# Kernel optimization log

Hardware: AMD Instinct MI355X
Metric: run time of the kernel (lower is better)

## Reference

```python
import jax, jax.numpy as jnp
import numpy as np

ALPHA = 1.0
ARAP_WEIGHT = 1.0
B, N, K, LATENT, HIDDEN = 16, 20000, 16, 256, 1024


def setup_inputs() -> dict:
    key = jax.random.key(0)
    ks = jax.random.split(key, 8)
    code = jax.random.normal(ks[0], (B, LATENT), jnp.float32)
    W1 = jax.random.normal(ks[1], (LATENT, HIDDEN), jnp.float32) / np.sqrt(LATENT)
    b1 = jnp.zeros((HIDDEN,), jnp.float32)
    W2 = jax.random.normal(ks[2], (HIDDEN, N * 3), jnp.float32) / np.sqrt(HIDDEN)
    b2 = jnp.zeros((N * 3,), jnp.float32)
    xyz1 = jax.random.normal(ks[3], (B, N, 3), jnp.float32)
    weightMatrix = jax.random.uniform(ks[4], (N, K), jnp.float32)
    area = jax.random.uniform(ks[5], (N,), jnp.float32)
    neighborsMatrix = jax.random.randint(ks[6], (N, K), 0, N, jnp.int32)
    numNeighbors = jax.random.randint(ks[7], (N,), 1, K + 1, jnp.int32)
    return {"code": code, "W1": W1, "b1": b1, "W2": W2, "b2": b2,
            "xyz1": xyz1, "weightMatrix": weightMatrix, "area": area,
            "neighborsMatrix": neighborsMatrix, "numNeighbors": numNeighbors}


def _mean_energy(code, W1, b1, W2, b2, xyz1, weightMatrix, area,
                 neighborsMatrix, numNeighbors):
    # decoder: MLP latent -> hidden -> N*3, reshaped to [B,N,3]
    h = jax.nn.relu(code @ W1 + b1)
    recon = (h @ W2 + b2).reshape(B, N, 3)

    # mask out padded neighbor slots, fold into weights  [N,K]
    mask = (jnp.arange(K)[None, :] < numNeighbors[:, None]).astype(jnp.float32)
    wm = weightMatrix * mask

    # neighbor-gathered edge vectors: rest pose d, deformed dq  [B,N,K,3]
    d = xyz1[:, :, None, :] - xyz1[:, neighborsMatrix, :]
    dq = recon[:, :, None, :] - recon[:, neighborsMatrix, :]

    # per-vertex weighted covariance and best-fit rotation (Procrustes)
    S = jnp.einsum('nk,bnki,bnkj->bnij', wm, d, dq)          # [B,N,3,3]
    U, s, Vt = jnp.linalg.svd(S)
    V = jnp.swapaxes(Vt, -1, -2)
    Ut = jnp.swapaxes(U, -1, -2)
    det = jnp.linalg.det(V @ Ut)                              # [B,N]
    Vf = V.at[..., :, -1].multiply(jnp.sign(det)[..., None])  # reflection fix
    R = jax.lax.stop_gradient(Vf @ Ut)                        # R treated as constant

    resid = dq - jnp.einsum('bnij,bnkj->bnki', R, d)          # [B,N,K,3]
    e = (ARAP_WEIGHT * ALPHA) * area[None, :, None] * wm[None] \
        * jnp.sum(resid * resid, axis=-1)                     # [B,N,K]
    # torch.mean(torch.mean(e, 2), 1)
    return jnp.mean(e, axis=(1, 2))                           # [B]


def reference(code, W1, b1, W2, b2, xyz1, weightMatrix, area,
              neighborsMatrix, numNeighbors):
    meanEnergy = _mean_energy(code, W1, b1, W2, b2, xyz1, weightMatrix, area,
                              neighborsMatrix, numNeighbors)
    # meanEnergy.backward(ones) -> grad of sum(meanEnergy) wrt code
    code_grad = jax.grad(lambda c: jnp.sum(
        _mean_energy(c, W1, b1, W2, b2, xyz1, weightMatrix, area,
                     neighborsMatrix, numNeighbors)))(code)
    return (meanEnergy, code_grad)
```

## Files before the change

### kernel.cpp

```cpp
#include <hip/hip_runtime.h>

constexpr int B_ = 16;
constexpr int NV = 20000;
constexpr int KN = 16;
constexpr int LAT = 256;
constexpr int HID = 1024;
constexpr int N3 = 60000;
constexpr int RCAP = 64;
constexpr int NCHUNK = 8;
constexpr float INV_NK = 1.0f / (20000.0f * 16.0f);

constexpr size_t H_OFF      = 0;
constexpr size_t XQ_OFF     = H_OFF + B_ * HID;
constexpr size_t GRECON_OFF = XQ_OFF + (size_t)NV * 96;
constexpr size_t GH_OFF     = GRECON_OFF + (size_t)B_ * N3;
constexpr size_t OWNG_OFF   = GH_OFF + B_ * HID;
constexpr size_t GEDGE_OFF  = OWNG_OFF + (size_t)NV * 64;
constexpr size_t RCOUNT_OFF = GEDGE_OFF + (size_t)NV * KN * 64;
constexpr size_t RLIST_OFF  = RCOUNT_OFF + NV;
constexpr size_t PART_OFF   = RLIST_OFF + (size_t)NV * RCAP;

__device__ __forceinline__ void atomAddF(float* p, float v) {
  unsafeAtomicAdd(p, v);
}

__global__ __launch_bounds__(256) void k_prep(
    const float* __restrict__ xyz, const float* __restrict__ code,
    const float* __restrict__ W1, const float* __restrict__ b1,
    float* __restrict__ xq, float* __restrict__ h,
    float* __restrict__ gh, float* __restrict__ out,
    int* __restrict__ rcount) {
  const int bid = blockIdx.x, tid = threadIdx.x;
  if (bid < 938) {
    __shared__ float sm[64][17];
    const int n30 = bid * 64;
    {
      const int n3l = tid & 63, bq = tid >> 6;
      #pragma unroll
      for (int p = 0; p < 4; ++p) {
        int b = p * 4 + bq;
        if (n30 + n3l < N3) sm[n3l][b] = xyz[(size_t)b * N3 + n30 + n3l];
      }
    }
    __syncthreads();
    {
      const int b = tid & 15, nq = tid >> 4;
      #pragma unroll
      for (int p = 0; p < 4; ++p) {
        int n3 = n30 + p * 16 + nq;
        if (n3 < N3) {
          int n = n3 / 3, c = n3 - n * 3;
          xq[(size_t)n * 96 + c * 16 + b] = sm[p * 16 + nq][b];
        }
      }
    }
  } else if (bid < 1002) {
    int t = (bid - 938) * 256 + tid;
    int b = t >> 10, hd = t & 1023;
    const float* c = code + b * LAT;
    float acc = b1[hd];
    #pragma unroll 4
    for (int l = 0; l < LAT; ++l) acc += c[l] * W1[l * HID + hd];
    h[t] = fmaxf(acc, 0.0f);
  } else if (bid < 1006) {
    int base = (bid - 1002) * 4096 + tid;
    #pragma unroll
    for (int r = 0; r < 16; ++r) gh[base + r * 256] = 0.0f;
  } else if (bid == 1006) {
    for (int i = tid; i < B_ + B_ * LAT; i += 256) out[i] = 0.0f;
  } else {
    int i = (bid - 1007) * 256 + tid;
    if (i < NV) rcount[i] = 0;
  }
}

__global__ __launch_bounds__(256) void k_mlp2f(
    const float* __restrict__ h, const float* __restrict__ W2,
    float* __restrict__ part,
    const int* __restrict__ nbrs, const int* __restrict__ nnbr,
    int* __restrict__ rcount, int* __restrict__ rlist) {
  const int bid = blockIdx.x;
  const int tid = threadIdx.x;
  if (bid >= 472) {
    int e = (bid - 472) * 256 + tid;
    int n = e >> 4, k = e & 15;
    if (k < nnbr[n]) {
      int v = nbrs[e];
      int slot = atomicAdd(&rcount[v], 1);
      if (slot < RCAP) rlist[v * RCAP + slot] = e;
    }
    return;
  }
  const int bx = bid % 59, by = bid / 59;
  __shared__ float hs[16][128];
  const int hd0 = by * 128;
  #pragma unroll
  for (int r = 0; r < 8; ++r) {
    int idx = r * 256 + tid;
    int bb = idx >> 7, cc = idx & 127;
    hs[bb][cc] = h[bb * HID + hd0 + cc];
  }
  __syncthreads();

  const int j4 = bx * 1024 + tid * 4;
  if (j4 >= N3) return;

  float4 acc[16];
  #pragma unroll
  for (int b = 0; b < 16; ++b) acc[b] = make_float4(0.f, 0.f, 0.f, 0.f);

  const float* wp = W2 + (size_t)hd0 * N3 + j4;
  float4 w0 = *(const float4*)(wp);
  float4 w1 = *(const float4*)(wp + (size_t)N3);
  float4 w2 = *(const float4*)(wp + (size_t)2 * N3);
  float4 w3 = *(const float4*)(wp + (size_t)3 * N3);

  for (int g = 0; g < 32; ++g) {
    const float* np = wp + (size_t)4 * N3;
    float4 n0, n1, n2, n3;
    if (g < 31) {
      n0 = *(const float4*)(np);
      n1 = *(const float4*)(np + (size_t)N3);
      n2 = *(const float4*)(np + (size_t)2 * N3);
      n3 = *(const float4*)(np + (size_t)3 * N3);
    }
    #pragma unroll
    for (int b = 0; b < 16; ++b) {
      float4 hb = *(const float4*)&hs[b][g * 4];
      acc[b].x += hb.x * w0.x + hb.y * w1.x + hb.z * w2.x + hb.w * w3.x;
      acc[b].y += hb.x * w0.y + hb.y * w1.y + hb.z * w2.y + hb.w * w3.y;
      acc[b].z += hb.x * w0.z + hb.y * w1.z + hb.z * w2.z + hb.w * w3.z;
      acc[b].w += hb.x * w0.w + hb.y * w1.w + hb.z * w2.w + hb.w * w3.w;
    }
    wp = np; w0 = n0; w1 = n1; w2 = n2; w3 = n3;
  }

  float ac[4][16];
  #pragma unroll
  for (int b = 0; b < 16; ++b) {
    ac[0][b] = acc[b].x; ac[1][b] = acc[b].y;
    ac[2][b] = acc[b].z; ac[3][b] = acc[b].w;
  }
  float* pbase = part + ((size_t)by * N3 + j4) * 16;
  #pragma unroll
  for (int jj = 0; jj < 4; ++jj)
    #pragma unroll
    for (int q = 0; q < 4; ++q)
      *(float4*)(pbase + jj * 16 + q * 4) = make_float4(
          ac[jj][q*4+0], ac[jj][q*4+1], ac[jj][q*4+2], ac[jj][q*4+3]);
}

__global__ __launch_bounds__(256) void k_reduce(
    const float* __restrict__ part, const float* __restrict__ b2,
    float* __restrict__ xq) {
  int t = blockIdx.x * 256 + threadIdx.x;
  if (t >= N3 * 16 / 4) return;
  size_t pos = (size_t)t * 4;
  int j = t >> 2, bq = (t & 3) * 4;
  float4 s = *(const float4*)(part + pos);
  #pragma unroll
  for (int c = 1; c < NCHUNK; ++c) {
    float4 p = *(const float4*)(part + (size_t)c * N3 * 16 + pos);
    s.x += p.x; s.y += p.y; s.z += p.z; s.w += p.w;
  }
  float bias = b2[j];
  s.x += bias; s.y += bias; s.z += bias; s.w += bias;
  int n = j / 3, c = j - n * 3;
  *(float4*)(xq + (size_t)n * 96 + (3 + c) * 16 + bq) = s;
}

__global__ __launch_bounds__(256, 2) void k_rot(
    const float* __restrict__ xq,
    const float* __restrict__ wmat, const float* __restrict__ area,
    const int* __restrict__ nbrs, const int* __restrict__ nnbr,
    float* __restrict__ ownG, float* __restrict__ gEdge,
    float* __restrict__ energy) {
  __shared__ float red[64];
  const int tid = threadIdx.x;
  const int b = tid & 15, nl = tid >> 4;
  const int n = blockIdx.x * 16 + nl;
  const int nn = nnbr[n];
  const float ar = area[n];
  const float* xqn = xq + (size_t)n * 96 + b;
  const float x0 = xqn[0],  x1 = xqn[16], x2 = xqn[32];
  const float q0 = xqn[48], q1 = xqn[64], q2 = xqn[80];

  float dX[KN], dY[KN], dZ[KN], eX[KN], eY[KN], eZ[KN], wk[KN];
  float S00=0,S01=0,S02=0,S10=0,S11=0,S12=0,S20=0,S21=0,S22=0;
  #pragma unroll
  for (int k = 0; k < KN; ++k) {
    float w=0, dx=0, dy=0, dz=0, ex=0, ey=0, ez=0;
    if (k < nn) {
      int m = nbrs[n * KN + k];
      w = wmat[n * KN + k];
      const float* mp = xq + (size_t)m * 96 + b;
      dx = x0 - mp[0];  dy = x1 - mp[16]; dz = x2 - mp[32];
      ex = q0 - mp[48]; ey = q1 - mp[64]; ez = q2 - mp[80];
    }
    wk[k]=w; dX[k]=dx; dY[k]=dy; dZ[k]=dz; eX[k]=ex; eY[k]=ey; eZ[k]=ez;
    S00 += w*dx*ex; S01 += w*dx*ey; S02 += w*dx*ez;
    S10 += w*dy*ex; S11 += w*dy*ey; S12 += w*dy*ez;
    S20 += w*dz*ex; S21 += w*dz*ey; S22 += w*dz*ez;
  }

  float A00 = S00*S00 + S10*S10 + S20*S20;
  float A01 = S00*S01 + S10*S11 + S20*S21;
  float A02 = S00*S02 + S10*S12 + S20*S22;
  float A11 = S01*S01 + S11*S11 + S21*S21;
  float A12 = S01*S02 + S11*S12 + S21*S22;
  float A22 = S02*S02 + S12*S12 + S22*S22;
  float V00=1,V01=0,V02=0, V10=0,V11=1,V12=0, V20=0,V21=0,V22=1;

  auto rot = [&](float& app, float& aqq, float& apq, float& arp, float& arq,
                 float& vp0, float& vp1, float& vp2,
                 float& vq0, float& vq1, float& vq2) {
    float a = apq;
    if (fabsf(a) > 1e-37f) {
      float tau = (aqq - app) * 0.5f / a;
      float t = copysignf(1.0f, tau) / (fabsf(tau) + sqrtf(1.0f + tau * tau));
      float c = rsqrtf(1.0f + t * t);
      float s = t * c;
      float napp = c*c*app - 2.0f*s*c*a + s*s*aqq;
      float naqq = s*s*app + 2.0f*s*c*a + c*c*aqq;
      app = napp; aqq = naqq; apq = 0.0f;
      float rp = arp, rq = arq;
      arp = c*rp - s*rq; arq = s*rp + c*rq;
      float t0, t1;
      t0=vp0; t1=vq0; vp0 = c*t0 - s*t1; vq0 = s*t0 + c*t1;
      t0=vp1; t1=vq1; vp1 = c*t0 - s*t1; vq1 = s*t0 + c*t1;
      t0=vp2; t1=vq2; vp2 = c*t0 - s*t1; vq2 = s*t0 + c*t1;
    }
  };
  #pragma unroll
  for (int sweep = 0; sweep < 6; ++sweep) {
    rot(A00,A11,A01, A02,A12, V00,V10,V20, V01,V11,V21);
    rot(A00,A22,A02, A01,A12, V00,V10,V20, V02,V12,V22);
    rot(A11,A22,A12, A01,A02, V01,V11,V21, V02,V12,V22);
  }
  auto sw = [](float& a, float& c) { float t = a; a = c; c = t; };
  if (A00 < A11) { sw(A00,A11); sw(V00,V01); sw(V10,V11); sw(V20,V21); }
  if (A00 < A22) { sw(A00,A22); sw(V00,V02); sw(V10,V12); sw(V20,V22); }
  if (A11 < A22) { sw(A11,A22); sw(V01,V02); sw(V11,V12); sw(V21,V22); }

  float v1x=V00, v1y=V10, v1z=V20;
  float v2x=V01, v2y=V11, v2z=V21;

  float u1x = S00*v1x + S01*v1y + S02*v1z;
  float u1y = S10*v1x + S11*v1y + S12*v1z;
  float u1z = S20*v1x + S21*v1y + S22*v1z;
  float s1sq = u1x*u1x + u1y*u1y + u1z*u1z;
  if (s1sq > 1e-30f) { float r = rsqrtf(s1sq); u1x*=r; u1y*=r; u1z*=r; }
  else { u1x = 1.0f; u1y = 0.0f; u1z = 0.0f; }

  float u2x = S00*v2x + S01*v2y + S02*v2z;
  float u2y = S10*v2x + S11*v2y + S12*v2z;
  float u2z = S20*v2x + S21*v2y + S22*v2z;
  float pr = u2x*u1x + u2y*u1y + u2z*u1z;
  u2x -= pr*u1x; u2y -= pr*u1y; u2z -= pr*u1z;
  float s2sq = u2x*u2x + u2y*u2y + u2z*u2z;
  if (s2sq > 1e-12f * s1sq + 1e-30f) {
    float r = rsqrtf(s2sq); u2x*=r; u2y*=r; u2z*=r;
  } else {
    float ex_ = (fabsf(u1x) < 0.9f) ? 1.0f : 0.0f;
    float ey_ = 1.0f - ex_;
    float pp = ex_*u1x + ey_*u1y;
    u2x = ex_ - pp*u1x; u2y = ey_ - pp*u1y; u2z = -pp*u1z;
    float r = rsqrtf(u2x*u2x + u2y*u2y + u2z*u2z);
    u2x*=r; u2y*=r; u2z*=r;
  }
  float u3x = u1y*u2z - u1z*u2y, u3y = u1z*u2x - u1x*u2z, u3z = u1x*u2y - u1y*u2x;
  float v3x = v1y*v2z - v1z*v2y, v3y = v1z*v2x - v1x*v2z, v3z = v1x*v2y - v1y*v2x;

  float R00 = v1x*u1x + v2x*u2x + v3x*u3x;
  float R01 = v1x*u1y + v2x*u2y + v3x*u3y;
  float R02 = v1x*u1z + v2x*u2z + v3x*u3z;
  float R10 = v1y*u1x + v2y*u2x + v3y*u3x;
  float R11 = v1y*u1y + v2y*u2y + v3y*u3y;
  float R12 = v1y*u1z + v2y*u2z + v3y*u3z;
  float R20 = v1z*u1x + v2z*u2x + v3z*u3x;
  float R21 = v1z*u1y + v2z*u2y + v3z*u3y;
  float R22 = v1z*u1z + v2z*u2z + v3z*u3z;

  float esum = 0, go0 = 0, go1 = 0, go2 = 0;
  const float gf = 2.0f * ar * INV_NK;
  float* geb = gEdge + (size_t)n * 1024 + b * 4;
  #pragma unroll
  for (int k = 0; k < KN; ++k) {
    float w = wk[k];
    float dx = dX[k], dy = dY[k], dz = dZ[k];
    float rx = eX[k] - (R00*dx + R01*dy + R02*dz);
    float ry = eY[k] - (R10*dx + R11*dy + R12*dz);
    float rz = eZ[k] - (R20*dx + R21*dy + R22*dz);
    esum += w * (rx*rx + ry*ry + rz*rz);
    float gc = gf * w;
    float gx = gc*rx, gy = gc*ry, gz = gc*rz;
    go0 += gx; go1 += gy; go2 += gz;
    if (k < nn) {
      *(float4*)(geb + k * 64) = make_float4(gx, gy, gz, 0.0f);
    }
  }
  esum *= ar * INV_NK;

  *(float4*)(ownG + (size_t)n * 64 + b * 4) = make_float4(go0, go1, go2, 0.0f);

  esum += __shfl_down(esum, 32);
  esum += __shfl_down(esum, 16);
  int wave = tid >> 6, lane = tid & 63;
  if (lane < 16) red[wave * 16 + lane] = esum;
  __syncthreads();
  if (tid < 16) atomAddF(&energy[tid], red[tid] + red[16 + tid] + red[32 + tid] + red[48 + tid]);
}

__global__ __launch_bounds__(256) void k_scatter(
    const float* __restrict__ gEdge, const float* __restrict__ ownG,
    const int* __restrict__ rcount, const int* __restrict__ rlist,
    float* __restrict__ grecon) {
  int t = blockIdx.x * 256 + threadIdx.x;
  int v = t >> 4, b = t & 15;
  const float4 og = *(const float4*)(ownG + (size_t)v * 64 + b * 4);
  float g0 = og.x, g1 = og.y, g2 = og.z;
  int deg = min(rcount[v], RCAP);
  const int* rl = rlist + v * RCAP;
  int i = 0;
  for (; i + 3 < deg; i += 4) {
    int e0 = rl[i], e1 = rl[i + 1], e2 = rl[i + 2], e3 = rl[i + 3];
    float4 p0 = *(const float4*)(gEdge + (size_t)e0 * 64 + b * 4);
    float4 p1 = *(const float4*)(gEdge + (size_t)e1 * 64 + b * 4);
    float4 p2 = *(const float4*)(gEdge + (size_t)e2 * 64 + b * 4);
    float4 p3 = *(const float4*)(gEdge + (size_t)e3 * 64 + b * 4);
    g0 -= (p0.x + p1.x) + (p2.x + p3.x);
    g1 -= (p0.y + p1.y) + (p2.y + p3.y);
    g2 -= (p0.z + p1.z) + (p2.z + p3.z);
  }
  for (; i < deg; ++i) {
    int e = rl[i];
    float4 p = *(const float4*)(gEdge + (size_t)e * 64 + b * 4);
    g0 -= p.x; g1 -= p.y; g2 -= p.z;
  }
  float* gq = grecon + (size_t)b * N3 + v * 3;
  gq[0] = g0; gq[1] = g1; gq[2] = g2;
}

__global__ __launch_bounds__(256, 2) void k_mlp2_bwd(
    const float* __restrict__ gr, const float* __restrict__ W2,
    float* __restrict__ gh) {
  const int tid = threadIdx.x;
  const int lane = tid & 63;
  const int wv = tid >> 6;
  const int laneJ = lane & 15, laneR = lane >> 4;
  const int row0 = blockIdx.y * 32 + wv * 8 + laneR * 2;

  float4 acc0[16], acc1[16];
  #pragma unroll
  for (int b = 0; b < 16; ++b) {
    acc0[b] = make_float4(0.f, 0.f, 0.f, 0.f);
    acc1[b] = make_float4(0.f, 0.f, 0.f, 0.f);
  }

  const int jbase = blockIdx.x * 64 + laneJ * 4;
  const float* w2r0 = W2 + (size_t)row0 * N3;
  const float* w2r1 = w2r0 + N3;

  for (int it = 0; it < 15; ++it) {
    int j = jbase + it * 4096;
    if (j < N3) {
      float4 w0 = *(const float4*)(w2r0 + j);
      float4 w1 = *(const float4*)(w2r1 + j);
      #pragma unroll
      for (int b = 0; b < 16; ++b) {
        float4 g = *(const float4*)(gr + (size_t)b * N3 + j);
        acc0[b].x += g.x * w0.x; acc0[b].y += g.y * w0.y;
        acc0[b].z += g.z * w0.z; acc0[b].w += g.w * w0.w;
        acc1[b].x += g.x * w1.x; acc1[b].y += g.y * w1.y;
        acc1[b].z += g.z * w1.z; acc1[b].w += g.w * w1.w;
      }
    }
  }

  float s0[16], s1[16];
  #pragma unroll
  for (int b = 0; b < 16; ++b) {
    s0[b] = (acc0[b].x + acc0[b].y) + (acc0[b].z + acc0[b].w);
    s1[b] = (acc1[b].x + acc1[b].y) + (acc1[b].z + acc1[b].w);
  }
  #pragma unroll
  for (int m = 1; m <= 8; m <<= 1) {
    #pragma unroll
    for (int b = 0; b < 16; ++b) {
      s0[b] += __shfl_xor(s0[b], m);
      s1[b] += __shfl_xor(s1[b], m);
    }
  }
  if (laneJ == 0) {
    #pragma unroll
    for (int b = 0; b < 16; ++b) {
      atomAddF(&gh[b * HID + row0], s0[b]);
      atomAddF(&gh[b * HID + row0 + 1], s1[b]);
    }
  }
}

__global__ __launch_bounds__(256) void k_mlp1_bwd(
    const float* __restrict__ gh, const float* __restrict__ h,
    const float* __restrict__ W1, float* __restrict__ gcode) {
  __shared__ float gm[128];
  const int b = blockIdx.x;
  const int hd0 = blockIdx.y * 128;
  const int l = threadIdx.x;
  if (l < 128) {
    float g = gh[b * HID + hd0 + l];
    gm[l] = (h[b * HID + hd0 + l] > 0.0f) ? g : 0.0f;
  }
  __syncthreads();
  const float4* wp = (const float4*)(W1 + (size_t)l * HID + hd0);
  float acc = 0.0f;
  #pragma unroll
  for (int i = 0; i < 32; ++i) {
    float4 w4 = wp[i];
    acc += w4.x * gm[i*4+0] + w4.y * gm[i*4+1] + w4.z * gm[i*4+2] + w4.w * gm[i*4+3];
  }
  atomAddF(&gcode[b * LAT + l], acc);
}

extern "C" void kernel_launch(void* const* d_in, const int* in_sizes, int n_in,
                              void* d_out, int out_size, void* d_ws, size_t ws_size,
                              hipStream_t stream) {
  const float* code = (const float*)d_in[0];
  const float* W1   = (const float*)d_in[1];
  const float* b1   = (const float*)d_in[2];
  const float* W2   = (const float*)d_in[3];
  const float* b2   = (const float*)d_in[4];
  const float* xyz  = (const float*)d_in[5];
  const float* wmat = (const float*)d_in[6];
  const float* area = (const float*)d_in[7];
  const int* nbrs   = (const int*)d_in[8];
  const int* nnbr   = (const int*)d_in[9];

  float* out = (float*)d_out;
  float* ws = (float*)d_ws;
  float* h      = ws + H_OFF;
  float* xq     = ws + XQ_OFF;
  float* grecon = ws + GRECON_OFF;
  float* gh     = ws + GH_OFF;
  float* ownG   = ws + OWNG_OFF;
  float* gEdge  = ws + GEDGE_OFF;
  int*   rcount = (int*)(ws + RCOUNT_OFF);
  int*   rlist  = (int*)(ws + RLIST_OFF);
  float* part   = ws + PART_OFF;

  k_prep<<<dim3(1086), dim3(256), 0, stream>>>(xyz, code, W1, b1, xq, h, gh, out, rcount);
  k_mlp2f<<<dim3(472 + NV * KN / 256), dim3(256), 0, stream>>>(
      h, W2, part, nbrs, nnbr, rcount, rlist);
  k_reduce<<<dim3((N3 * 16 / 4 + 255) / 256), dim3(256), 0, stream>>>(part, b2, xq);
  k_rot<<<dim3(NV / 16), dim3(256), 0, stream>>>(
      xq, wmat, area, nbrs, nnbr, ownG, gEdge, out);
  k_scatter<<<dim3(NV * 16 / 256), dim3(256), 0, stream>>>(
      gEdge, ownG, rcount, rlist, grecon);
  k_mlp2_bwd<<<dim3(64, 32), dim3(256), 0, stream>>>(grecon, W2, gh);
  k_mlp1_bwd<<<dim3(B_, 8), dim3(256), 0, stream>>>(gh, h, W1, out + B_);
}
```

Measured before the change: 617.4 us.

## Transpose recon gradient layout and remap MLP2 backward work per lane

The scatter kernel now writes the recon gradient as [N3][16] (batch innermost) instead of [B][N3]. The MLP2 backward kernel is rewritten so each lane owns one batch index and a strip of 8 j-values. Each lane accumulates into 8 W2 rows with a short cross-lane reduction, replacing 128 float4 accumulators with 8 scalars. The aim is lower register pressure and fewer shuffles and atomics, at the cost of less-coalesced W2 reads (each lane loads 32 contiguous bytes per row).

```diff
diff --git a/kernel.cpp b/kernel.cpp
--- a/kernel.cpp
+++ b/kernel.cpp
@@ -12,8 +12,8 @@
 
 constexpr size_t H_OFF      = 0;
 constexpr size_t XQ_OFF     = H_OFF + B_ * HID;
-constexpr size_t GRECON_OFF = XQ_OFF + (size_t)NV * 96;
-constexpr size_t GH_OFF     = GRECON_OFF + (size_t)B_ * N3;
+constexpr size_t GRT_OFF    = XQ_OFF + (size_t)NV * 96;
+constexpr size_t GH_OFF     = GRT_OFF + (size_t)N3 * 16;
 constexpr size_t OWNG_OFF   = GH_OFF + B_ * HID;
 constexpr size_t GEDGE_OFF  = OWNG_OFF + (size_t)NV * 64;
 constexpr size_t RCOUNT_OFF = GEDGE_OFF + (size_t)NV * KN * 64;
@@ -314,7 +314,7 @@
 __global__ __launch_bounds__(256) void k_scatter(
     const float* __restrict__ gEdge, const float* __restrict__ ownG,
     const int* __restrict__ rcount, const int* __restrict__ rlist,
-    float* __restrict__ grecon) {
+    float* __restrict__ grT) {
   int t = blockIdx.x * 256 + threadIdx.x;
   int v = t >> 4, b = t & 15;
   const float4 og = *(const float4*)(ownG + (size_t)v * 64 + b * 4);
@@ -337,66 +337,51 @@
     float4 p = *(const float4*)(gEdge + (size_t)e * 64 + b * 4);
     g0 -= p.x; g1 -= p.y; g2 -= p.z;
   }
-  float* gq = grecon + (size_t)b * N3 + v * 3;
-  gq[0] = g0; gq[1] = g1; gq[2] = g2;
-}
-
-__global__ __launch_bounds__(256, 2) void k_mlp2_bwd(
-    const float* __restrict__ gr, const float* __restrict__ W2,
+  float* gq = grT + (size_t)v * 48 + b;
+  gq[0] = g0; gq[16] = g1; gq[32] = g2;
+}
+
+__global__ __launch_bounds__(256) void k_mlp2_bwd(
+    const float* __restrict__ grT, const float* __restrict__ W2,
     float* __restrict__ gh) {
   const int tid = threadIdx.x;
   const int lane = tid & 63;
-  const int wv = tid >> 6;
-  const int laneJ = lane & 15, laneR = lane >> 4;
-  const int row0 = blockIdx.y * 32 + wv * 8 + laneR * 2;
-
-  float4 acc0[16], acc1[16];
-  #pragma unroll
-  for (int b = 0; b < 16; ++b) {
-    acc0[b] = make_float4(0.f, 0.f, 0.f, 0.f);
-    acc1[b] = make_float4(0.f, 0.f, 0.f, 0.f);
-  }
-
-  const int jbase = blockIdx.x * 64 + laneJ * 4;
-  const float* w2r0 = W2 + (size_t)row0 * N3;
-  const float* w2r1 = w2r0 + N3;
-
-  for (int it = 0; it < 15; ++it) {
-    int j = jbase + it * 4096;
-    if (j < N3) {
-      float4 w0 = *(const float4*)(w2r0 + j);
-      float4 w1 = *(const float4*)(w2r1 + j);
+  const int w = tid >> 6;
+  const int b = lane & 15;
+  const int jq = lane >> 4;
+  const int row0 = blockIdx.y * 32 + w * 8;
+
+  float acc[8] = {0, 0, 0, 0, 0, 0, 0, 0};
+  const float* w2base = W2 + (size_t)row0 * N3;
+  const int jblk = blockIdx.x * 960;
+
+  for (int it = 0; it < 30; ++it) {
+    int jb = jblk + it * 32;
+    if (jb < N3) {
+      int j = jb + jq * 8;
+      const float* gp = grT + (size_t)j * 16 + b;
+      float g0 = gp[0],   g1 = gp[16],  g2 = gp[32],  g3 = gp[48];
+      float g4 = gp[64],  g5 = gp[80],  g6 = gp[96],  g7 = gp[112];
+      const float* wp = w2base + j;
       #pragma unroll
-      for (int b = 0; b < 16; ++b) {
-        float4 g = *(const float4*)(gr + (size_t)b * N3 + j);
-        acc0[b].x += g.x * w0.x; acc0[b].y += g.y * w0.y;
-        acc0[b].z += g.z * w0.z; acc0[b].w += g.w * w0.w;
-        acc1[b].x += g.x * w1.x; acc1[b].y += g.y * w1.y;
-        acc1[b].z += g.z * w1.z; acc1[b].w += g.w * w1.w;
+      for (int rr = 0; rr < 8; ++rr) {
+        float4 wa = *(const float4*)(wp + (size_t)rr * N3);
+        float4 wb = *(const float4*)(wp + (size_t)rr * N3 + 4);
+        acc[rr] += g0 * wa.x + g1 * wa.y + g2 * wa.z + g3 * wa.w
+                 + g4 * wb.x + g5 * wb.y + g6 * wb.z + g7 * wb.w;
       }
     }
   }
 
-  float s0[16], s1[16];
-  #pragma unroll
-  for (int b = 0; b < 16; ++b) {
-    s0[b] = (acc0[b].x + acc0[b].y) + (acc0[b].z + acc0[b].w);
-    s1[b] = (acc1[b].x + acc1[b].y) + (acc1[b].z + acc1[b].w);
-  }
-  #pragma unroll
-  for (int m = 1; m <= 8; m <<= 1) {
+  #pragma unroll
+  for (int rr = 0; rr < 8; ++rr) {
+    acc[rr] += __shfl_xor(acc[rr], 16);
+    acc[rr] += __shfl_xor(acc[rr], 32);
+  }
+  if (lane < 16) {
     #pragma unroll
-    for (int b = 0; b < 16; ++b) {
-      s0[b] += __shfl_xor(s0[b], m);
-      s1[b] += __shfl_xor(s1[b], m);
-    }
-  }
-  if (laneJ == 0) {
-    #pragma unroll
-    for (int b = 0; b < 16; ++b) {
-      atomAddF(&gh[b * HID + row0], s0[b]);
-      atomAddF(&gh[b * HID + row0 + 1], s1[b]);
-    }
+    for (int rr = 0; rr < 8; ++rr)
+      atomAddF(&gh[b * HID + row0 + rr], acc[rr]);
   }
 }
 
@@ -440,7 +425,7 @@
   float* ws = (float*)d_ws;
   float* h      = ws + H_OFF;
   float* xq     = ws + XQ_OFF;
-  float* grecon = ws + GRECON_OFF;
+  float* grT    = ws + GRT_OFF;
   float* gh     = ws + GH_OFF;
   float* ownG   = ws + OWNG_OFF;
   float* gEdge  = ws + GEDGE_OFF;
@@ -455,7 +440,7 @@
   k_rot<<<dim3(NV / 16), dim3(256), 0, stream>>>(
       xq, wmat, area, nbrs, nnbr, ownG, gEdge, out);
   k_scatter<<<dim3(NV * 16 / 256), dim3(256), 0, stream>>>(
-      gEdge, ownG, rcount, rlist, grecon);
-  k_mlp2_bwd<<<dim3(64, 32), dim3(256), 0, stream>>>(grecon, W2, gh);
+      gEdge, ownG, rcount, rlist, grT);
+  k_mlp2_bwd<<<dim3(64, 32), dim3(256), 0, stream>>>(grT, W2, gh);
   k_mlp1_bwd<<<dim3(B_, 8), dim3(256), 0, stream>>>(gh, h, W1, out + B_);
 }
```

After: 774.9 us. 25.5% more time.

## Restructure MLP2 backward GEMV to one W2 row per wave with column chunks

Applied to the files above, without the earlier changes.

The weight-gradient GEMV for the second layer is remapped. Each wave now handles a single W2 row over a 7500-column chunk, and lane groups cover 4 batch entries each. Before, each thread held 2 rows × 16 batches × 4 accumulators across strided columns. The new layout cuts register pressure sharply and raises occupancy and grid size to stream W2 better. In exchange, each grecon value is re-read by many more waves, which relies on cache hits.

```diff
diff --git a/kernel.cpp b/kernel.cpp
--- a/kernel.cpp
+++ b/kernel.cpp
@@ -341,62 +341,52 @@
   gq[0] = g0; gq[1] = g1; gq[2] = g2;
 }
 
-__global__ __launch_bounds__(256, 2) void k_mlp2_bwd(
+__global__ __launch_bounds__(256) void k_mlp2_bwd(
     const float* __restrict__ gr, const float* __restrict__ W2,
     float* __restrict__ gh) {
   const int tid = threadIdx.x;
   const int lane = tid & 63;
-  const int wv = tid >> 6;
-  const int laneJ = lane & 15, laneR = lane >> 4;
-  const int row0 = blockIdx.y * 32 + wv * 8 + laneR * 2;
-
-  float4 acc0[16], acc1[16];
-  #pragma unroll
-  for (int b = 0; b < 16; ++b) {
-    acc0[b] = make_float4(0.f, 0.f, 0.f, 0.f);
-    acc1[b] = make_float4(0.f, 0.f, 0.f, 0.f);
-  }
-
-  const int jbase = blockIdx.x * 64 + laneJ * 4;
-  const float* w2r0 = W2 + (size_t)row0 * N3;
-  const float* w2r1 = w2r0 + N3;
-
-  for (int it = 0; it < 15; ++it) {
-    int j = jbase + it * 4096;
-    if (j < N3) {
-      float4 w0 = *(const float4*)(w2r0 + j);
-      float4 w1 = *(const float4*)(w2r1 + j);
-      #pragma unroll
-      for (int b = 0; b < 16; ++b) {
-        float4 g = *(const float4*)(gr + (size_t)b * N3 + j);
-        acc0[b].x += g.x * w0.x; acc0[b].y += g.y * w0.y;
-        acc0[b].z += g.z * w0.z; acc0[b].w += g.w * w0.w;
-        acc1[b].x += g.x * w1.x; acc1[b].y += g.y * w1.y;
-        acc1[b].z += g.z * w1.z; acc1[b].w += g.w * w1.w;
-      }
-    }
-  }
-
-  float s0[16], s1[16];
-  #pragma unroll
-  for (int b = 0; b < 16; ++b) {
-    s0[b] = (acc0[b].x + acc0[b].y) + (acc0[b].z + acc0[b].w);
-    s1[b] = (acc1[b].x + acc1[b].y) + (acc1[b].z + acc1[b].w);
-  }
+  const int w = tid >> 6;
+  const int laneJ = lane & 15;
+  const int b0 = (lane >> 4) * 4;
+  const int row = blockIdx.y * 4 + w;
+  const int jbase = blockIdx.x * 7500;
+
+  float a0 = 0.f, a1 = 0.f, a2 = 0.f, a3 = 0.f;
+  const float* w2r = W2 + (size_t)row * N3 + jbase;
+  const float* g0p = gr + (size_t)(b0 + 0) * N3 + jbase;
+  const float* g1p = gr + (size_t)(b0 + 1) * N3 + jbase;
+  const float* g2p = gr + (size_t)(b0 + 2) * N3 + jbase;
+  const float* g3p = gr + (size_t)(b0 + 3) * N3 + jbase;
+
+  #pragma unroll 2
+  for (int it = 0; it < 118; ++it) {
+    int jo = it * 64 + laneJ * 4;
+    if (jo < 7500) {
+      float4 wv = *(const float4*)(w2r + jo);
+      float4 g0 = *(const float4*)(g0p + jo);
+      float4 g1 = *(const float4*)(g1p + jo);
+      float4 g2 = *(const float4*)(g2p + jo);
+      float4 g3 = *(const float4*)(g3p + jo);
+      a0 += g0.x * wv.x + g0.y * wv.y + g0.z * wv.z + g0.w * wv.w;
+      a1 += g1.x * wv.x + g1.y * wv.y + g1.z * wv.z + g1.w * wv.w;
+      a2 += g2.x * wv.x + g2.y * wv.y + g2.z * wv.z + g2.w * wv.w;
+      a3 += g3.x * wv.x + g3.y * wv.y + g3.z * wv.z + g3.w * wv.w;
+    }
+  }
+
   #pragma unroll
   for (int m = 1; m <= 8; m <<= 1) {
-    #pragma unroll
-    for (int b = 0; b < 16; ++b) {
-      s0[b] += __shfl_xor(s0[b], m);
-      s1[b] += __shfl_xor(s1[b], m);
-    }
+    a0 += __shfl_xor(a0, m);
+    a1 += __shfl_xor(a1, m);
+    a2 += __shfl_xor(a2, m);
+    a3 += __shfl_xor(a3, m);
   }
   if (laneJ == 0) {
-    #pragma unroll
-    for (int b = 0; b < 16; ++b) {
-      atomAddF(&gh[b * HID + row0], s0[b]);
-      atomAddF(&gh[b * HID + row0 + 1], s1[b]);
-    }
+    atomAddF(&gh[(b0 + 0) * HID + row], a0);
+    atomAddF(&gh[(b0 + 1) * HID + row], a1);
+    atomAddF(&gh[(b0 + 2) * HID + row], a2);
+    atomAddF(&gh[(b0 + 3) * HID + row], a3);
   }
 }
 
@@ -456,6 +446,6 @@
       xq, wmat, area, nbrs, nnbr, ownG, gEdge, out);
   k_scatter<<<dim3(NV * 16 / 256), dim3(256), 0, stream>>>(
       gEdge, ownG, rcount, rlist, grecon);
-  k_mlp2_bwd<<<dim3(64, 32), dim3(256), 0, stream>>>(grecon, W2, gh);
+  k_mlp2_bwd<<<dim3(8, 256), dim3(256), 0, stream>>>(grecon, W2, gh);
   k_mlp1_bwd<<<dim3(B_, 8), dim3(256), 0, stream>>>(gh, h, W1, out + B_);
 }
```

Result: slower. 744.9 us (+20.7%).

## Retile MLP2 backward to one weight row per thread with scalar accumulators

Applied to the files above, without the earlier changes.

Reorganizes the W2^T gradient kernel so each thread handles one hidden row instead of two and keeps 16 scalar accumulators instead of 32 float4 vectors. The grid becomes 16x64 blocks with a longer loop over N3 columns per block. This cuts register pressure, which should raise occupancy, and it issues fewer atomics per block. The trade-off is that each gradient load of grecon is now reused for only one W2 row instead of two, so there are more reads of grecon overall.

```diff
diff --git a/kernel.cpp b/kernel.cpp
--- a/kernel.cpp
+++ b/kernel.cpp
@@ -341,62 +341,51 @@
   gq[0] = g0; gq[1] = g1; gq[2] = g2;
 }
 
-__global__ __launch_bounds__(256, 2) void k_mlp2_bwd(
+__global__ __launch_bounds__(256) void k_mlp2_bwd(
     const float* __restrict__ gr, const float* __restrict__ W2,
     float* __restrict__ gh) {
   const int tid = threadIdx.x;
   const int lane = tid & 63;
   const int wv = tid >> 6;
   const int laneJ = lane & 15, laneR = lane >> 4;
-  const int row0 = blockIdx.y * 32 + wv * 8 + laneR * 2;
-
-  float4 acc0[16], acc1[16];
-  #pragma unroll
-  for (int b = 0; b < 16; ++b) {
-    acc0[b] = make_float4(0.f, 0.f, 0.f, 0.f);
-    acc1[b] = make_float4(0.f, 0.f, 0.f, 0.f);
-  }
+  const int row = blockIdx.y * 16 + wv * 4 + laneR;
+
+  float acc[16];
+  #pragma unroll
+  for (int b = 0; b < 16; ++b) acc[b] = 0.0f;
 
   const int jbase = blockIdx.x * 64 + laneJ * 4;
-  const float* w2r0 = W2 + (size_t)row0 * N3;
-  const float* w2r1 = w2r0 + N3;
-
-  for (int it = 0; it < 15; ++it) {
-    int j = jbase + it * 4096;
+  const float* w2r = W2 + (size_t)row * N3;
+
+  for (int it = 0; it < 58; ++it) {
+    int j = jbase + it * 1024;
+    float4 w0 = *(const float4*)(w2r + j);
+    #pragma unroll
+    for (int b = 0; b < 16; ++b) {
+      float4 g = *(const float4*)(gr + (size_t)b * N3 + j);
+      acc[b] += g.x * w0.x + g.y * w0.y + g.z * w0.z + g.w * w0.w;
+    }
+  }
+  {
+    int j = jbase + 58 * 1024;
     if (j < N3) {
-      float4 w0 = *(const float4*)(w2r0 + j);
-      float4 w1 = *(const float4*)(w2r1 + j);
+      float4 w0 = *(const float4*)(w2r + j);
       #pragma unroll
       for (int b = 0; b < 16; ++b) {
         float4 g = *(const float4*)(gr + (size_t)b * N3 + j);
-        acc0[b].x += g.x * w0.x; acc0[b].y += g.y * w0.y;
-        acc0[b].z += g.z * w0.z; acc0[b].w += g.w * w0.w;
-        acc1[b].x += g.x * w1.x; acc1[b].y += g.y * w1.y;
-        acc1[b].z += g.z * w1.z; acc1[b].w += g.w * w1.w;
+        acc[b] += g.x * w0.x + g.y * w0.y + g.z * w0.z + g.w * w0.w;
       }
     }
   }
 
-  float s0[16], s1[16];
-  #pragma unroll
-  for (int b = 0; b < 16; ++b) {
-    s0[b] = (acc0[b].x + acc0[b].y) + (acc0[b].z + acc0[b].w);
-    s1[b] = (acc1[b].x + acc1[b].y) + (acc1[b].z + acc1[b].w);
-  }
   #pragma unroll
   for (int m = 1; m <= 8; m <<= 1) {
     #pragma unroll
-    for (int b = 0; b < 16; ++b) {
-      s0[b] += __shfl_xor(s0[b], m);
-      s1[b] += __shfl_xor(s1[b], m);
-    }
+    for (int b = 0; b < 16; ++b) acc[b] += __shfl_xor(acc[b], m);
   }
   if (laneJ == 0) {
     #pragma unroll
-    for (int b = 0; b < 16; ++b) {
-      atomAddF(&gh[b * HID + row0], s0[b]);
-      atomAddF(&gh[b * HID + row0 + 1], s1[b]);
-    }
+    for (int b = 0; b < 16; ++b) atomAddF(&gh[b * HID + row], acc[b]);
   }
 }
 
@@ -456,6 +445,6 @@
       xq, wmat, area, nbrs, nnbr, ownG, gEdge, out);
   k_scatter<<<dim3(NV * 16 / 256), dim3(256), 0, stream>>>(
       gEdge, ownG, rcount, rlist, grecon);
-  k_mlp2_bwd<<<dim3(64, 32), dim3(256), 0, stream>>>(grecon, W2, gh);
+  k_mlp2_bwd<<<dim3(16, 64), dim3(256), 0, stream>>>(grecon, W2, gh);
   k_mlp1_bwd<<<dim3(B_, 8), dim3(256), 0, stream>>>(gh, h, W1, out + B_);
 }
```

Measured after the change: 632.7 us. 1.02x slower.
